# Kernel optimization log

Hardware: AMD Instinct MI355X
Metric: run time of the kernel (lower is better)

## Reference

```python
import jax, jax.numpy as jnp
import numpy as np
from jax import lax

# Static config (matches init_kwargs / electrode montage)
B, T, V = 16, 1536, 64
F1, D, H = 16, 2, 4
F2 = F1 * D              # 32
FO = F2 // H             # 8, GAT per-head out dim
K1, K3 = 32, 16          # conv kernel sizes (temporal)
P1, P2 = 8, 4            # avg pool sizes
KNN = 4
EPS = 1e-5
NEG_SLOPE = 0.2          # PyG GATConv leaky_relu slope


def _build_edges():
    # deterministic electrode geometry -> kNN graph, plus PyG self-loops
    rng = np.random.RandomState(0)
    pos = rng.randn(V, 3)
    dmat = np.linalg.norm(pos[:, None] - pos[None, :], axis=-1)
    order = np.argsort(dmat, axis=1)
    nbrs = order[:, 1:KNN + 1]                      # exclude self
    src = np.repeat(np.arange(V), KNN)
    dst = nbrs.reshape(-1)
    # add self loops (GATConv default add_self_loops=True)
    src = np.concatenate([src, np.arange(V)])
    dst = np.concatenate([dst, np.arange(V)])
    return jnp.asarray(np.stack([src, dst]), dtype=jnp.int32)  # (2, E)


def _bn(x, g, b, m, v, axis):
    shp = [1] * x.ndim
    shp[axis] = -1
    rs = lambda a: a.reshape(shp)
    return rs(g) * (x - rs(m)) * lax.rsqrt(rs(v) + EPS) + rs(b)


def _conv_same_t(x, w, k):
    # Conv2d(..., (1,k), padding='same'): torch pads (k-1)//2 left, rest right
    lp = (k - 1) // 2
    return lax.conv_general_dilated(x, w, (1, 1), [(0, 0), (lp, k - 1 - lp)],
                                    dimension_numbers=('NCHW', 'OIHW', 'NCHW'))


def _gat(x, W, a_src, a_dst, bias, src, dst):
    # Batched PyG GATConv (eval mode, dropout off), concat heads.
    # x: (Ng, V, F1); W: (F1, H*FO); a_src/a_dst: (H, FO); bias: (H*FO,)
    Ng = x.shape[0]
    h = jnp.einsum('nvf,fho->nvho', x, W.reshape(F1, H, FO))   # (Ng,V,H,FO)
    es = jnp.einsum('nvho,ho->nvh', h, a_src)[:, src]          # (Ng,E,H)
    ed = jnp.einsum('nvho,ho->nvh', h, a_dst)[:, dst]
    e = jax.nn.leaky_relu(es + ed, NEG_SLOPE)
    # softmax over incoming edges of each target node (segment softmax)
    m = jnp.full((Ng, V, H), -1e30, e.dtype).at[:, dst].max(e)
    ex = jnp.exp(e - m[:, dst])
    den = jnp.zeros((Ng, V, H), e.dtype).at[:, dst].add(ex)
    alpha = ex / den[:, dst]                                   # (Ng,E,H)
    out = jnp.zeros((Ng, V, H, FO), e.dtype).at[:, dst].add(alpha[..., None] * h[:, src])
    return out.reshape(Ng, V, H * FO) + bias


def setup_inputs() -> dict:
    key = jax.random.key(0)
    ks = jax.random.split(key, 16)
    bn = lambda k, c: (1.0 + 0.1 * jax.random.normal(jax.random.fold_in(k, 0), (c,)),
                       0.1 * jax.random.normal(jax.random.fold_in(k, 1), (c,)),
                       0.1 * jax.random.normal(jax.random.fold_in(k, 2), (c,)),
                       0.5 + jax.random.uniform(jax.random.fold_in(k, 3), (c,)))
    bn1 = bn(ks[1], F1); bn2 = bn(ks[2], F2); bn3 = bn(ks[3], F2)
    inp = {
        'x': jax.random.normal(ks[0], (B, 1, V, T), jnp.float32),
        'conv1_w': 0.1 * jax.random.normal(ks[4], (F1, 1, 1, K1), jnp.float32),
        'bn1_g': bn1[0], 'bn1_b': bn1[1], 'bn1_m': bn1[2], 'bn1_v': bn1[3],
        'gat_w': (1.0 / np.sqrt(F1)) * jax.random.normal(ks[5], (F1, H * FO), jnp.float32),
        'gat_asrc': 0.3 * jax.random.normal(ks[6], (H, FO), jnp.float32),
        'gat_adst': 0.3 * jax.random.normal(ks[7], (H, FO), jnp.float32),
        'gat_bias': 0.05 * jax.random.normal(ks[8], (H * FO,), jnp.float32),
        'bn2_g': bn2[0], 'bn2_b': bn2[1], 'bn2_m': bn2[2], 'bn2_v': bn2[3],
        'conv3_w': 0.1 * jax.random.normal(ks[9], (F2, F2, 1, K3), jnp.float32),
        'bn3_g': bn3[0], 'bn3_b': bn3[1], 'bn3_m': bn3[2], 'bn3_v': bn3[3],
        'edge_index': _build_edges(),
    }
    return inp


def reference(x, conv1_w, bn1_g, bn1_b, bn1_m, bn1_v,
              gat_w, gat_asrc, gat_adst, gat_bias,
              bn2_g, bn2_b, bn2_m, bn2_v,
              conv3_w, bn3_g, bn3_b, bn3_m, bn3_v, edge_index):
    src, dst = edge_index[0], edge_index[1]
    # block1: temporal conv + BN
    h = _conv_same_t(x, conv1_w, K1)                 # (B,F1,V,T)
    h = _bn(h, bn1_g, bn1_b, bn1_m, bn1_v, 1)
    # spatial GNN over B*T independent electrode graphs
    xg = h.transpose(0, 3, 2, 1).reshape(B * T, V, F1)
    g = _gat(xg, gat_w, gat_asrc, gat_adst, gat_bias, src, dst)   # (BT,V,F2)
    g = g.mean(axis=1).reshape(B, T, F2).transpose(0, 2, 1)       # (B,F2,T)
    g = _bn(g, bn2_g, bn2_b, bn2_m, bn2_v, 1)[:, :, None, :]      # (B,F2,1,T)
    # tail: elu -> pool -> conv -> bn -> elu -> pool (dropout = eval no-op)
    h = jax.nn.elu(g)
    h = h.reshape(B, F2, 1, T // P1, P1).mean(-1)
    h = _conv_same_t(h, conv3_w, K3)
    h = _bn(h, bn3_g, bn3_b, bn3_m, bn3_v, 1)
    h = jax.nn.elu(h)
    h = h.reshape(B, F2, 1, T // P1 // P2, P2).mean(-1)           # (B,F2,1,48)
    return h
```

## Files before the change

kernel.cpp:

```cpp
#include <hip/hip_runtime.h>
#include <math.h>

#define TPB 256

constexpr int Bc = 16, Tc = 1536;
constexpr int T2c = 192;
constexpr float EPSc = 1e-5f;
constexpr float NSLOPE = 0.2f;
constexpr int MDI = 16;
constexpr int MDO = 8;
constexpr float L2E = 1.4426950408889634f;

typedef float vf2 __attribute__((ext_vector_type(2)));

constexpr int OW_WEFF = 0;
constexpr int OW_CHL  = 1024;
constexpr int OW_CES  = 1056;
constexpr int OW_WES  = 1064;
constexpr int OW_WED  = 1192;
constexpr int OW_A2C2 = 1320;
constexpr int OW_WFT  = 1384;
constexpr int OW_GRAPH= 2408;
constexpr int OW_P    = 2825;

constexpr int GB_INTS = 417;

constexpr int L_XT  = 0;
constexpr int L_WB  = 2720;
constexpr int L_Y   = 4896;
constexpr int L_GR  = 6208;
constexpr int L_TOT = 6625;

#define LGKM0() __asm__ volatile("s_waitcnt lgkmcnt(0)" ::: "memory")

__device__ __forceinline__ int xt_idx(int row, int g, int lo)
{
    return L_XT + row * 68 + (((g + row) & 15) << 2) + lo;
}

__device__ __forceinline__ float lexp2(float z)
{
    return __builtin_amdgcn_exp2f(fmaxf(z, NSLOPE * z));
}

__device__ __forceinline__ float bfly16_sum(float s)
{
#if __has_builtin(__builtin_amdgcn_permlane16_swap)
    unsigned u = __builtin_bit_cast(unsigned, s);
    auto r = __builtin_amdgcn_permlane16_swap(u, u, false, false);
    return __builtin_bit_cast(float, (unsigned)r[0]) +
           __builtin_bit_cast(float, (unsigned)r[1]);
#else
    return s + __shfl_xor(s, 16);
#endif
}

__device__ __forceinline__ float bfly32_sum(float s)
{
#if __has_builtin(__builtin_amdgcn_permlane32_swap)
    unsigned u = __builtin_bit_cast(unsigned, s);
    auto r = __builtin_amdgcn_permlane32_swap(u, u, false, false);
    return __builtin_bit_cast(float, (unsigned)r[0]) +
           __builtin_bit_cast(float, (unsigned)r[1]);
#else
    return s + __shfl_xor(s, 32);
#endif
}

__global__ void prep_kernel(const float* __restrict__ c1w,
                            const float* __restrict__ g1, const float* __restrict__ b1,
                            const float* __restrict__ m1, const float* __restrict__ v1,
                            const float* __restrict__ W,
                            const float* __restrict__ asrc, const float* __restrict__ adst,
                            const float* __restrict__ bias,
                            const float* __restrict__ g2, const float* __restrict__ b2,
                            const float* __restrict__ m2, const float* __restrict__ v2,
                            const int* __restrict__ ei, int ne, float* __restrict__ ws)
{
    const int tid = threadIdx.x;
    __shared__ float sweff[1024];
    __shared__ float schl[32];
    __shared__ int isrcp_i[64 * MDI];
    __shared__ int outdst_i[64 * MDO];
    __shared__ int inslot[64], outslot[64];

    for (int idx = tid; idx < 1024; idx += TPB) {
        int k = idx >> 5, f2 = idx & 31;
        float s = 0.f;
        for (int f = 0; f < 16; f++) {
            float a1 = g1[f] * rsqrtf(v1[f] + EPSc);
            s += a1 * W[f * 32 + f2] * c1w[f * 32 + k];
        }
        ws[OW_WEFF + idx] = s;
        ws[OW_WFT + f2 * 32 + k] = s;
        sweff[idx] = s;
    }
    for (int f2 = tid; f2 < 32; f2 += TPB) {
        float s = 0.f;
        for (int f = 0; f < 16; f++) {
            float a1 = g1[f] * rsqrtf(v1[f] + EPSc);
            s = fmaf(b1[f] - a1 * m1[f], W[f * 32 + f2], s);
        }
        ws[OW_CHL + f2] = s;
        schl[f2] = s;
        float a2 = g2[f2] * rsqrtf(v2[f2] + EPSc);
        ws[OW_A2C2 + f2] = a2;
        ws[OW_A2C2 + 32 + f2] = b2[f2] + a2 * (bias[f2] - m2[f2]);
    }

    for (int i = tid; i < 64 * MDI; i += TPB) isrcp_i[i] = 0;
    for (int i = tid; i < 64 * MDO; i += TPB) outdst_i[i] = 0;
    if (tid < 64) { inslot[tid] = 0; outslot[tid] = 0; }
    __syncthreads();
    for (int e = tid; e < ne; e += TPB) {
        int s = ei[e], d = ei[ne + e];
        if (s == d) continue;
        int pi = atomicAdd(&inslot[d], 1);
        if (pi < 15) isrcp_i[d * MDI + pi] = s;
        int po = atomicAdd(&outslot[s], 1);
        if (po < MDO) outdst_i[s * MDO + po] = d;
    }
    __syncthreads();

    if (tid < 128) {
        int k = tid >> 2, h = tid & 3;
        float s1 = 0.f, s2 = 0.f;
        for (int o = 0; o < 8; o++) {
            float wv = sweff[k * 32 + h * 8 + o];
            s1 = fmaf(asrc[h * 8 + o], wv, s1);
            s2 = fmaf(adst[h * 8 + o], wv, s2);
        }
        ws[OW_WES + h * 32 + k] = s1;
        ws[OW_WED + h * 32 + k] = s2;
    }
    if (tid < 4) {
        float s1 = 0.f, s2 = 0.f;
        for (int o = 0; o < 8; o++) {
            float cv = schl[tid * 8 + o];
            s1 = fmaf(asrc[tid * 8 + o], cv, s1);
            s2 = fmaf(adst[tid * 8 + o], cv, s2);
        }
        ws[OW_CES + tid] = s1;
        ws[OW_CES + 4 + tid] = s2;
    }
    unsigned char* gb = (unsigned char*)(ws + OW_GRAPH);
    for (int i = tid; i < 64 * MDI; i += TPB) gb[i] = (unsigned char)isrcp_i[i];
    for (int i = tid; i < 64 * MDO; i += TPB) gb[1088 + i] = (unsigned char)outdst_i[i];
    __syncthreads();
    if (tid < 64) {
        int id = inslot[tid] < 15 ? inslot[tid] : 15;
        int od = outslot[tid] < MDO ? outslot[tid] : MDO;
        gb[tid * MDI + 15] = (unsigned char)id;
        gb[1024 + tid] = (unsigned char)id;
        gb[1600 + tid] = (unsigned char)od;
    }
    __syncthreads();
    if (tid == 0) {
        int mi = 0;
        for (int d = 0; d < 64; d++) {
            int a = gb[1024 + d];
            mi = a > mi ? a : mi;
        }
        gb[1664] = (unsigned char)mi;
        gb[1665] = 0;
    }
}

__global__ __launch_bounds__(TPB, 4) void gat_kernel(
    const float* __restrict__ x,
    const float* __restrict__ wfTp,
    const float* __restrict__ chlp,
    const float* __restrict__ cesg,
    const float* __restrict__ wesg,
    const float* __restrict__ wedg,
    const float* __restrict__ a2c2,
    const int* __restrict__ graphi,
    float* __restrict__ pout)
{
    __shared__ __align__(16) float sm[L_TOT];
    unsigned char* gb = (unsigned char*)&sm[L_GR];

    const int tid  = threadIdx.x;
    const int b    = blockIdx.x / 192;
    const int tile = blockIdx.x % 192;
    const int t0   = tile * 8;

    const int h = tid >> 6, v = tid & 63;

    for (int idx = tid; idx < GB_INTS; idx += TPB) ((int*)&sm[L_GR])[idx] = graphi[idx];
    for (int idx = tid; idx < 2560; idx += TPB) {
        const int vv = idx / 40, j = idx % 40;
        float val = 1.0f;
        if (j < 39) {
            const int t = t0 - 15 + j;
            val = (t >= 0 && t < Tc) ? x[(b * 64 + vv) * Tc + t] : 0.f;
        }
        sm[xt_idx(j, vv >> 2, vv & 3)] = val;
    }
    __syncthreads();

    const int hs = __builtin_amdgcn_readfirstlane(h);
    const float* wesh = wesg + hs * 32;
    const float* wedh = wedg + hs * 32;

    float aes[8], aed[8];
    {
        const int g = v >> 2, lo = v & 3;
        const float cesh = cesg[hs], cedh = cesg[4 + hs];
        #pragma unroll
        for (int t = 0; t < 8; t++) { aes[t] = cesh; aed[t] = cedh; }
        float xr[8];
        #pragma unroll
        for (int q = 0; q < 7; q++) xr[q] = sm[xt_idx(q, g, lo)];
        #pragma unroll
        for (int k = 0; k < 32; k++) {
            xr[(k + 7) & 7] = sm[xt_idx(k + 7, g, lo)];
            const float wek = wesh[k];
            const float wdk = wedh[k];
            #pragma unroll
            for (int t = 0; t < 8; t++) {
                const float xv = xr[(k + t) & 7];
                aes[t] = fmaf(xv, wek, aes[t]);
                aed[t] = fmaf(xv, wdk, aed[t]);
            }
        }
        #pragma unroll
        for (int t = 0; t < 8; t++) { aes[t] *= L2E; aed[t] *= L2E; }
    }

    {
        float* esL = &sm[L_Y + h * 328];

        const int4 il = *(const int4*)(gb + v * MDI);
        const unsigned ow = *(const unsigned*)(gb + 1088 + v * MDO);
        const int indeg = (int)(((unsigned)il.w) >> 24);
        const int mdin = __builtin_amdgcn_readfirstlane((int)gb[1664]);
        const unsigned iw[4] = {(unsigned)il.x, (unsigned)il.y,
                                (unsigned)il.z, (unsigned)il.w};

        float den[8], Eself[8];
        #pragma unroll
        for (int t = 0; t < 8; t++) {
            Eself[t] = lexp2(aes[t] + aed[t]);
            den[t] = Eself[t];
        }

        #pragma unroll
        for (int hf = 0; hf < 2; hf++) {
            *(float4*)(esL + v * 4) = (float4){aes[hf * 4 + 0], aes[hf * 4 + 1],
                                              aes[hf * 4 + 2], aes[hf * 4 + 3]};
            LGKM0();
            #pragma unroll
            for (int e = 0; e < 15; e++) {
                if (e < mdin) {
                    const int s = (int)((iw[e >> 2] >> ((e & 3) * 8)) & 0xFF);
                    const float4 e4 = *(const float4*)(esL + s * 4);
                    const float valid = (e < indeg) ? 1.f : 0.f;
                    den[hf * 4 + 0] += valid * lexp2(e4.x + aed[hf * 4 + 0]);
                    den[hf * 4 + 1] += valid * lexp2(e4.y + aed[hf * 4 + 1]);
                    den[hf * 4 + 2] += valid * lexp2(e4.z + aed[hf * 4 + 2]);
                    den[hf * 4 + 3] += valid * lexp2(e4.w + aed[hf * 4 + 3]);
                }
            }
            LGKM0();
        }

        float rden[8], wb[8];
        #pragma unroll
        for (int t = 0; t < 8; t++) {
            float r = __builtin_amdgcn_rcpf(den[t]);
            r = r * (2.f - den[t] * r);
            rden[t] = r;
            wb[t] = Eself[t] * r;
        }

        #pragma unroll
        for (int qt = 0; qt < 4; qt++) {
            *(float4*)(esL + v * 4) = (float4){aed[2 * qt], aed[2 * qt + 1],
                                               rden[2 * qt], rden[2 * qt + 1]};
            LGKM0();
            #pragma unroll
            for (int j = 0; j < 4; j++) {
                const int d = (int)((ow >> (j * 8)) & 0xFF);
                const float4 g4 = *(const float4*)(esL + d * 4);
                wb[2 * qt + 0] = fmaf(lexp2(aes[2 * qt + 0] + g4.x), g4.z, wb[2 * qt + 0]);
                wb[2 * qt + 1] = fmaf(lexp2(aes[2 * qt + 1] + g4.y), g4.w, wb[2 * qt + 1]);
            }
            LGKM0();
        }

        #pragma unroll
        for (int t = 0; t < 8; t++)
            sm[L_WB + h * 544 + t * 68 + v] = wb[t];
    }
    LGKM0();

    {
        const int cg = v & 7;
        const int th = (v >> 3) & 1;
        const int kq = v >> 4;

        vf2 yp[4][5];
        #pragma unroll
        for (int i = 0; i < 4; i++)
            #pragma unroll
            for (int q = 0; q < 5; q++) yp[i][q] = (vf2){0.f, 0.f};

        const float* wbbase = &sm[L_WB + h * 544 + (th * 4) * 68];
        #pragma unroll
        for (int v4 = 0; v4 < 4; v4++) {
            const int vcol = kq * 16 + v4 * 4;
            float4 wrow[4];
            #pragma unroll
            for (int i = 0; i < 4; i++)
                wrow[i] = *(const float4*)(wbbase + i * 68 + vcol);
            #pragma unroll
            for (int q = 0; q < 5; q++) {
                const int row = cg * 5 + q;
                const int mg = ((kq * 4 + v4 + row) & 15) << 2;
                const float4 x4 = *(const float4*)(&sm[L_XT + row * 68 + mg]);
                const vf2 x01 = (vf2){x4.x, x4.y}, x23 = (vf2){x4.z, x4.w};
                #pragma unroll
                for (int i = 0; i < 4; i++) {
                    const vf2 w01 = (vf2){wrow[i].x, wrow[i].y};
                    const vf2 w23 = (vf2){wrow[i].z, wrow[i].w};
                    yp[i][q] += w01 * x01;
                    yp[i][q] += w23 * x23;
                }
            }
        }
        float ya[4][5];
        #pragma unroll
        for (int i = 0; i < 4; i++)
            #pragma unroll
            for (int q = 0; q < 5; q++) {
                float s = yp[i][q].x + yp[i][q].y;
                ya[i][q] = bfly32_sum(bfly16_sum(s));
            }
        float* yw = &sm[L_Y + h * 328 + (th * 4 + kq) * 41 + cg * 5];
        #pragma unroll
        for (int q = 0; q < 5; q++) {
            float a01 = (kq & 1) ? ya[1][q] : ya[0][q];
            float a23 = (kq & 1) ? ya[3][q] : ya[2][q];
            yw[q] = (kq & 2) ? a23 : a01;
        }
    }
    LGKM0();

    {
        const int t = v >> 3, o = v & 7;
        const int f2d = h * 8 + o;
        const float4* wf4 = (const float4*)(wfTp + f2d * 32);

        const float* yr = &sm[L_Y + h * 328 + t * 41];
        float acc = chlp[f2d] * yr[39];
        #pragma unroll
        for (int k4 = 0; k4 < 8; k4++) {
            const float4 w = wf4[k4];
            acc = fmaf(w.x, yr[t + 4 * k4 + 0],
                  fmaf(w.y, yr[t + 4 * k4 + 1],
                  fmaf(w.z, yr[t + 4 * k4 + 2],
                  fmaf(w.w, yr[t + 4 * k4 + 3], acc))));
        }

        const float a2 = a2c2[f2d], c2 = a2c2[32 + f2d];
        float y = fmaf(a2, acc * (1.f / 64.f), c2);
        y = y > 0.f ? y : __expf(y) - 1.f;
        y += __shfl_xor(y, 8);
        y = bfly32_sum(bfly16_sum(y));
        if (v < 8)
            pout[(b * T2c + tile) * 32 + h * 8 + v] = y * 0.125f;
    }
}

__global__ __launch_bounds__(TPB) void conv3_kernel(const float* __restrict__ pp,
                                                    const float* __restrict__ w3,
                                                    const float* __restrict__ g3,
                                                    const float* __restrict__ b3,
                                                    const float* __restrict__ m3,
                                                    const float* __restrict__ v3,
                                                    float* __restrict__ outp)
{
    __shared__ float pl[63 * 32];
    __shared__ float q[48 * 32];
    const int tid = threadIdx.x;
    const int b = blockIdx.x >> 2, cc = blockIdx.x & 3;

    for (int idx = tid; idx < 63 * 32; idx += TPB) {
        int r = idx >> 5, f2 = idx & 31;
        int tog = cc * 48 - 7 + r;
        pl[idx] = (tog >= 0 && tog < T2c) ? pp[(b * T2c + tog) * 32 + f2] : 0.f;
    }
    __syncthreads();

    const int f2o = tid & 31, grp = tid >> 5;
    const int tb = grp * 6;
    float acc[6] = { 0.f, 0.f, 0.f, 0.f, 0.f, 0.f };
    for (int f2i = 0; f2i < 32; f2i++) {
        float seg[21];
        #pragma unroll
        for (int r = 0; r < 21; r++) seg[r] = pl[(tb + r) * 32 + f2i];
        const float4* wrow = (const float4*)(w3 + (f2o * 32 + f2i) * 16);
        #pragma unroll
        for (int k4 = 0; k4 < 4; k4++) {
            const float4 w4 = wrow[k4];
            #pragma unroll
            for (int j = 0; j < 6; j++) {
                acc[j] = fmaf(seg[j + k4 * 4 + 0], w4.x,
                         fmaf(seg[j + k4 * 4 + 1], w4.y,
                         fmaf(seg[j + k4 * 4 + 2], w4.z,
                         fmaf(seg[j + k4 * 4 + 3], w4.w, acc[j]))));
            }
        }
    }
    const float a3 = g3[f2o] * rsqrtf(v3[f2o] + EPSc);
    const float c3 = b3[f2o] - a3 * m3[f2o];
    #pragma unroll
    for (int j = 0; j < 6; j++) {
        float y = fmaf(a3, acc[j], c3);
        y = y > 0.f ? y : __expf(y) - 1.f;
        q[(tb + j) * 32 + f2o] = y;
    }
    __syncthreads();
    for (int idx = tid; idx < 12 * 32; idx += TPB) {
        int t4 = idx >> 5, f2 = idx & 31;
        int r0 = t4 * 4;
        float s = q[r0 * 32 + f2] + q[(r0 + 1) * 32 + f2] +
                  q[(r0 + 2) * 32 + f2] + q[(r0 + 3) * 32 + f2];
        outp[(b * 32 + f2) * 48 + cc * 12 + t4] = s * 0.25f;
    }
}

extern "C" void kernel_launch(void* const* d_in, const int* in_sizes, int n_in,
                              void* d_out, int out_size, void* d_ws, size_t ws_size,
                              hipStream_t stream)
{
    const float* x    = (const float*)d_in[0];
    const float* c1w  = (const float*)d_in[1];
    const float* g1   = (const float*)d_in[2];
    const float* b1   = (const float*)d_in[3];
    const float* m1   = (const float*)d_in[4];
    const float* v1   = (const float*)d_in[5];
    const float* W    = (const float*)d_in[6];
    const float* asrc = (const float*)d_in[7];
    const float* adst = (const float*)d_in[8];
    const float* bias = (const float*)d_in[9];
    const float* g2   = (const float*)d_in[10];
    const float* b2   = (const float*)d_in[11];
    const float* m2   = (const float*)d_in[12];
    const float* v2   = (const float*)d_in[13];
    const float* w3   = (const float*)d_in[14];
    const float* g3   = (const float*)d_in[15];
    const float* b3   = (const float*)d_in[16];
    const float* m3   = (const float*)d_in[17];
    const float* v3   = (const float*)d_in[18];
    const int*   ei   = (const int*)d_in[19];
    const int    ne   = in_sizes[19] / 2;

    float* ws = (float*)d_ws;

    prep_kernel<<<1, TPB, 0, stream>>>(c1w, g1, b1, m1, v1, W, asrc, adst,
                                       bias, g2, b2, m2, v2, ei, ne, ws);

    gat_kernel<<<Bc * T2c, TPB, 0, stream>>>(x,
                                             ws + OW_WFT, ws + OW_CHL,
                                             ws + OW_CES,
                                             ws + OW_WES, ws + OW_WED,
                                             ws + OW_A2C2,
                                             (const int*)(ws + OW_GRAPH),
                                             ws + OW_P);

    conv3_kernel<<<Bc * 4, TPB, 0, stream>>>(ws + OW_P, w3, g3, b3, m3, v3,
                                             (float*)d_out);
}
```

Baseline: 166.0 us.

## Pack src/dst attention weights, fold bias constant, read graph from global, widen LDS passes

```diff
diff --git a/kernel.cpp b/kernel.cpp
--- a/kernel.cpp
+++ b/kernel.cpp
@@ -16,20 +16,17 @@
 constexpr int OW_WEFF = 0;
 constexpr int OW_CHL  = 1024;
 constexpr int OW_CES  = 1056;
-constexpr int OW_WES  = 1064;
-constexpr int OW_WED  = 1192;
+constexpr int OW_WSD  = 1064;
 constexpr int OW_A2C2 = 1320;
 constexpr int OW_WFT  = 1384;
 constexpr int OW_GRAPH= 2408;
 constexpr int OW_P    = 2825;
 
-constexpr int GB_INTS = 417;
 
 constexpr int L_XT  = 0;
 constexpr int L_WB  = 2720;
 constexpr int L_Y   = 4896;
-constexpr int L_GR  = 6208;
-constexpr int L_TOT = 6625;
+constexpr int L_TOT = 6208;
 
 #define LGKM0() __asm__ volatile("s_waitcnt lgkmcnt(0)" ::: "memory")
 
@@ -105,7 +102,7 @@
         schl[f2] = s;
         float a2 = g2[f2] * rsqrtf(v2[f2] + EPSc);
         ws[OW_A2C2 + f2] = a2;
-        ws[OW_A2C2 + 32 + f2] = b2[f2] + a2 * (bias[f2] - m2[f2]);
+        ws[OW_A2C2 + 32 + f2] = b2[f2] + a2 * (bias[f2] - m2[f2] + s);
     }
 
     for (int i = tid; i < 64 * MDI; i += TPB) isrcp_i[i] = 0;
@@ -130,8 +127,8 @@
             s1 = fmaf(asrc[h * 8 + o], wv, s1);
             s2 = fmaf(adst[h * 8 + o], wv, s2);
         }
-        ws[OW_WES + h * 32 + k] = s1;
-        ws[OW_WED + h * 32 + k] = s2;
+        ws[OW_WSD + h * 64 + k * 2]     = s1;
+        ws[OW_WSD + h * 64 + k * 2 + 1] = s2;
     }
     if (tid < 4) {
         float s1 = 0.f, s2 = 0.f;
@@ -140,8 +137,8 @@
             s1 = fmaf(asrc[tid * 8 + o], cv, s1);
             s2 = fmaf(adst[tid * 8 + o], cv, s2);
         }
-        ws[OW_CES + tid] = s1;
-        ws[OW_CES + 4 + tid] = s2;
+        ws[OW_CES + tid * 2]     = s1;
+        ws[OW_CES + tid * 2 + 1] = s2;
     }
     unsigned char* gb = (unsigned char*)(ws + OW_GRAPH);
     for (int i = tid; i < 64 * MDI; i += TPB) gb[i] = (unsigned char)isrcp_i[i];
@@ -169,16 +166,13 @@
 __global__ __launch_bounds__(TPB, 4) void gat_kernel(
     const float* __restrict__ x,
     const float* __restrict__ wfTp,
-    const float* __restrict__ chlp,
     const float* __restrict__ cesg,
-    const float* __restrict__ wesg,
-    const float* __restrict__ wedg,
+    const float* __restrict__ wsdg,
     const float* __restrict__ a2c2,
     const int* __restrict__ graphi,
     float* __restrict__ pout)
 {
     __shared__ __align__(16) float sm[L_TOT];
-    unsigned char* gb = (unsigned char*)&sm[L_GR];
 
     const int tid  = threadIdx.x;
     const int b    = blockIdx.x / 192;
@@ -187,7 +181,11 @@
 
     const int h = tid >> 6, v = tid & 63;
 
-    for (int idx = tid; idx < GB_INTS; idx += TPB) ((int*)&sm[L_GR])[idx] = graphi[idx];
+    const unsigned char* gbg = (const unsigned char*)graphi;
+    const int4 il = *(const int4*)(gbg + v * MDI);
+    const unsigned ow = *(const unsigned*)(gbg + 1088 + v * MDO);
+    const int mdin = __builtin_amdgcn_readfirstlane(((const int*)graphi)[416] & 0xFF);
+
     for (int idx = tid; idx < 2560; idx += TPB) {
         const int vv = idx / 40, j = idx % 40;
         float val = 1.0f;
@@ -200,41 +198,40 @@
     __syncthreads();
 
     const int hs = __builtin_amdgcn_readfirstlane(h);
-    const float* wesh = wesg + hs * 32;
-    const float* wedh = wedg + hs * 32;
+    const vf2* wsdh = (const vf2*)(wsdg + hs * 64);
 
     float aes[8], aed[8];
     {
         const int g = v >> 2, lo = v & 3;
-        const float cesh = cesg[hs], cedh = cesg[4 + hs];
-        #pragma unroll
-        for (int t = 0; t < 8; t++) { aes[t] = cesh; aed[t] = cedh; }
+        const vf2 cv = *(const vf2*)(cesg + hs * 2);
+        vf2 acc2[8];
+        #pragma unroll
+        for (int t = 0; t < 8; t++) acc2[t] = cv;
         float xr[8];
         #pragma unroll
         for (int q = 0; q < 7; q++) xr[q] = sm[xt_idx(q, g, lo)];
         #pragma unroll
         for (int k = 0; k < 32; k++) {
             xr[(k + 7) & 7] = sm[xt_idx(k + 7, g, lo)];
-            const float wek = wesh[k];
-            const float wdk = wedh[k];
+            const vf2 wk = wsdh[k];
             #pragma unroll
             for (int t = 0; t < 8; t++) {
                 const float xv = xr[(k + t) & 7];
-                aes[t] = fmaf(xv, wek, aes[t]);
-                aed[t] = fmaf(xv, wdk, aed[t]);
-            }
-        }
-        #pragma unroll
-        for (int t = 0; t < 8; t++) { aes[t] *= L2E; aed[t] *= L2E; }
+                acc2[t] += (vf2){xv, xv} * wk;
+            }
+        }
+        #pragma unroll
+        for (int t = 0; t < 8; t++) {
+            aes[t] = acc2[t].x * L2E;
+            aed[t] = acc2[t].y * L2E;
+        }
     }
 
     {
-        float* esL = &sm[L_Y + h * 328];
-
-        const int4 il = *(const int4*)(gb + v * MDI);
-        const unsigned ow = *(const unsigned*)(gb + 1088 + v * MDO);
+        float* esL0 = &sm[L_Y + h * 328];
+        float* esL1 = &sm[L_WB + h * 544];
+
         const int indeg = (int)(((unsigned)il.w) >> 24);
-        const int mdin = __builtin_amdgcn_readfirstlane((int)gb[1664]);
         const unsigned iw[4] = {(unsigned)il.x, (unsigned)il.y,
                                 (unsigned)il.z, (unsigned)il.w};
 
@@ -245,25 +242,27 @@
             den[t] = Eself[t];
         }
 
-        #pragma unroll
-        for (int hf = 0; hf < 2; hf++) {
-            *(float4*)(esL + v * 4) = (float4){aes[hf * 4 + 0], aes[hf * 4 + 1],
-                                              aes[hf * 4 + 2], aes[hf * 4 + 3]};
-            LGKM0();
-            #pragma unroll
-            for (int e = 0; e < 15; e++) {
-                if (e < mdin) {
-                    const int s = (int)((iw[e >> 2] >> ((e & 3) * 8)) & 0xFF);
-                    const float4 e4 = *(const float4*)(esL + s * 4);
-                    const float valid = (e < indeg) ? 1.f : 0.f;
-                    den[hf * 4 + 0] += valid * lexp2(e4.x + aed[hf * 4 + 0]);
-                    den[hf * 4 + 1] += valid * lexp2(e4.y + aed[hf * 4 + 1]);
-                    den[hf * 4 + 2] += valid * lexp2(e4.z + aed[hf * 4 + 2]);
-                    den[hf * 4 + 3] += valid * lexp2(e4.w + aed[hf * 4 + 3]);
-                }
-            }
-            LGKM0();
-        }
+        *(float4*)(esL0 + v * 4) = (float4){aes[0], aes[1], aes[2], aes[3]};
+        *(float4*)(esL1 + v * 4) = (float4){aes[4], aes[5], aes[6], aes[7]};
+        LGKM0();
+        #pragma unroll
+        for (int e = 0; e < 15; e++) {
+            if (e < mdin) {
+                const int s = (int)((iw[e >> 2] >> ((e & 3) * 8)) & 0xFF);
+                const float4 ea = *(const float4*)(esL0 + s * 4);
+                const float4 eb = *(const float4*)(esL1 + s * 4);
+                const float valid = (e < indeg) ? 1.f : 0.f;
+                den[0] += valid * lexp2(ea.x + aed[0]);
+                den[1] += valid * lexp2(ea.y + aed[1]);
+                den[2] += valid * lexp2(ea.z + aed[2]);
+                den[3] += valid * lexp2(ea.w + aed[3]);
+                den[4] += valid * lexp2(eb.x + aed[4]);
+                den[5] += valid * lexp2(eb.y + aed[5]);
+                den[6] += valid * lexp2(eb.z + aed[6]);
+                den[7] += valid * lexp2(eb.w + aed[7]);
+            }
+        }
+        LGKM0();
 
         float rden[8], wb[8];
         #pragma unroll
@@ -275,16 +274,22 @@
         }
 
         #pragma unroll
-        for (int qt = 0; qt < 4; qt++) {
-            *(float4*)(esL + v * 4) = (float4){aed[2 * qt], aed[2 * qt + 1],
-                                               rden[2 * qt], rden[2 * qt + 1]};
+        for (int hf = 0; hf < 2; hf++) {
+            const int tb4 = hf * 4;
+            *(float4*)(esL0 + v * 4) = (float4){aed[tb4 + 0], aed[tb4 + 1],
+                                                rden[tb4 + 0], rden[tb4 + 1]};
+            *(float4*)(esL1 + v * 4) = (float4){aed[tb4 + 2], aed[tb4 + 3],
+                                                rden[tb4 + 2], rden[tb4 + 3]};
             LGKM0();
             #pragma unroll
             for (int j = 0; j < 4; j++) {
                 const int d = (int)((ow >> (j * 8)) & 0xFF);
-                const float4 g4 = *(const float4*)(esL + d * 4);
-                wb[2 * qt + 0] = fmaf(lexp2(aes[2 * qt + 0] + g4.x), g4.z, wb[2 * qt + 0]);
-                wb[2 * qt + 1] = fmaf(lexp2(aes[2 * qt + 1] + g4.y), g4.w, wb[2 * qt + 1]);
+                const float4 g0 = *(const float4*)(esL0 + d * 4);
+                const float4 g1 = *(const float4*)(esL1 + d * 4);
+                wb[tb4 + 0] = fmaf(lexp2(aes[tb4 + 0] + g0.x), g0.z, wb[tb4 + 0]);
+                wb[tb4 + 1] = fmaf(lexp2(aes[tb4 + 1] + g0.y), g0.w, wb[tb4 + 1]);
+                wb[tb4 + 2] = fmaf(lexp2(aes[tb4 + 2] + g1.x), g1.z, wb[tb4 + 2]);
+                wb[tb4 + 3] = fmaf(lexp2(aes[tb4 + 3] + g1.y), g1.w, wb[tb4 + 3]);
             }
             LGKM0();
         }
@@ -353,7 +358,7 @@
         const float4* wf4 = (const float4*)(wfTp + f2d * 32);
 
         const float* yr = &sm[L_Y + h * 328 + t * 41];
-        float acc = chlp[f2d] * yr[39];
+        float acc = 0.f;
         #pragma unroll
         for (int k4 = 0; k4 < 8; k4++) {
             const float4 w = wf4[k4];
@@ -463,9 +468,9 @@
                                        bias, g2, b2, m2, v2, ei, ne, ws);
 
     gat_kernel<<<Bc * T2c, TPB, 0, stream>>>(x,
-                                             ws + OW_WFT, ws + OW_CHL,
+                                             ws + OW_WFT,
                                              ws + OW_CES,
-                                             ws + OW_WES, ws + OW_WED,
+                                             ws + OW_WSD,
                                              ws + OW_A2C2,
                                              (const int*)(ws + OW_GRAPH),
                                              ws + OW_P);
```

Result: faster. 161.2 us (-2.9%).
